# Performance work log

Measured on AMD Instinct MI355X. Metric: run time of the kernel, lower is better.

## Reference

```python
import jax, jax.numpy as jnp
import numpy as np

B, D, C, H, L = 32768, 64, 64, 1024, 6
EPS = 1e-5
NIN = (D - D // 2) + C  # unchanged half + cond = 96
SPLIT = D // 2          # 32


def setup_inputs() -> dict:
    key = jax.random.key(0)
    ks = jax.random.split(key, 12)
    s = 0.05
    return {
        "z": jax.random.normal(ks[0], (B, D), jnp.float32),
        "cond": jax.random.normal(ks[1], (B, C), jnp.float32),
        "W1": jax.random.normal(ks[2], (L, NIN, H), jnp.float32) * s,
        "b1": jax.random.normal(ks[3], (L, H), jnp.float32) * s,
        "W2": jax.random.normal(ks[4], (L, H, H), jnp.float32) * s,
        "b2": jax.random.normal(ks[5], (L, H), jnp.float32) * s,
        "Ws": jax.random.normal(ks[6], (L, H, SPLIT), jnp.float32) * s,
        "bs": jax.random.normal(ks[7], (L, SPLIT), jnp.float32) * s,
        "Wt": jax.random.normal(ks[8], (L, H, SPLIT), jnp.float32) * s,
        "bt": jax.random.normal(ks[9], (L, SPLIT), jnp.float32) * s,
        "bn_w": 1.0 + 0.1 * jax.random.normal(ks[10], (L, D), jnp.float32),
        "bn_b": 0.1 * jax.random.normal(ks[11], (L, D), jnp.float32),
    }


def reference(z, cond, W1, b1, W2, b2, Ws, bs, Wt, bt, bn_w, bn_b):
    x = z
    log_det = jnp.zeros((z.shape[0],), z.dtype)
    for i in range(L):
        # 'even' mask keeps even indices on even layers, odd indices otherwise
        if i % 2 == 0:
            keep, chg = np.arange(0, D, 2), np.arange(1, D, 2)
        else:
            keep, chg = np.arange(1, D, 2), np.arange(0, D, 2)
        # 2-layer MLP on [x_keep, cond]
        h = jax.nn.relu(jnp.concatenate([x[:, keep], cond], axis=1) @ W1[i] + b1[i])
        h = jax.nn.relu(h @ W2[i] + b2[i])
        log_s = jnp.tanh(h @ Ws[i] + bs[i])          # (B, SPLIT)
        t = h @ Wt[i] + bt[i]                         # (B, SPLIT)
        x2t = x[:, chg] * jnp.exp(log_s) + t
        x = jnp.zeros_like(x).at[:, keep].set(x[:, keep]).at[:, chg].set(x2t)
        log_det = log_det + log_s.sum(axis=1)
        # BatchNorm1d, training mode: batch mean / biased variance, eps=1e-5
        mean = x.mean(axis=0)
        var = x.var(axis=0)
        x = (x - mean) * jax.lax.rsqrt(var + EPS) * bn_w[i] + bn_b[i]
        log_det = log_det + jnp.log(jnp.abs(bn_w[i])).sum()
    return x, log_det
```

## Files before the change

### kernel.cpp

```cpp
#include <hip/hip_runtime.h>
#include <math.h>

#define BB 32768
#define DD 64
#define CC 64
#define HH 1024
#define LL 6
#define SPLIT 32
#define NIN 96
#define EPSV 1e-5f

typedef short short8 __attribute__((ext_vector_type(8)));
typedef float f32x4 __attribute__((ext_vector_type(4)));
typedef unsigned short u16;

__device__ __forceinline__ u16 f2bf(float f) {
    union { float f; unsigned int u; } c; c.f = f;
    unsigned int u = c.u + 0x7FFFu + ((c.u >> 16) & 1u);
    return (u16)(u >> 16);
}

__device__ __forceinline__ void gl_lds16(const u16* g, u16* l) {
    __builtin_amdgcn_global_load_lds(
        (const __attribute__((address_space(1))) unsigned int*)g,
        (__attribute__((address_space(3))) unsigned int*)l, 16, 0, 0);
}

__global__ void transpose_cvt_kernel(const float* __restrict__ src, u16* __restrict__ dst,
                                     int R, int C, int Rpad,
                                     long long sstride, long long dstride)
{
    __shared__ float tile[32][33];
    const float* s = src + (size_t)blockIdx.z * sstride;
    u16* d = dst + (size_t)blockIdx.z * dstride;
    int r0 = blockIdx.x * 32, c0 = blockIdx.y * 32;
    int tc = threadIdx.x & 31, tr = threadIdx.x >> 5;
#pragma unroll
    for (int i = 0; i < 4; ++i) {
        int r = r0 + tr + i * 8;
        tile[tr + i * 8][tc] = (r < R) ? s[(size_t)r * C + c0 + tc] : 0.f;
    }
    __syncthreads();
#pragma unroll
    for (int i = 0; i < 4; ++i) {
        int cc = tr + i * 8;
        d[(size_t)(c0 + cc) * Rpad + r0 + tc] = f2bf(tile[tc][cc]);
    }
}

__global__ __launch_bounds__(256)
void init_ain_cond_kernel(const float* __restrict__ cond, u16* __restrict__ Ain)
{
    int t = blockIdx.x * 256 + threadIdx.x;
    int c = t % 96, r = t / 96;
    Ain[(size_t)r * 128 + 32 + c] = (c < CC) ? f2bf(cond[(size_t)r * CC + c]) : (u16)0;
}

__global__ __launch_bounds__(256)
void build_keep_kernel(const float* __restrict__ x, u16* __restrict__ Ain, int keep_off)
{
    int t = blockIdx.x * 256 + threadIdx.x;
    int c = t & 31, r = t >> 5;
    Ain[(size_t)r * 128 + c] = f2bf(x[(size_t)r * DD + 2 * c + keep_off]);
}

__global__ __launch_bounds__(512, 2)
void gemm_tiled(const u16* __restrict__ A,
                const u16* __restrict__ Bt,
                const float* __restrict__ bias,
                u16* __restrict__ Cc,
                int K)
{
    __shared__ u16 sA[3][16 * 512];
    __shared__ u16 sB[3][16 * 512];

    const int t = threadIdx.x;
    const int w = t >> 6, lane = t & 63;
    const int lane16 = lane & 15, quad = lane >> 4;
    const int wm = w >> 2, wn = w & 3;

    int id = blockIdx.x;
    int nby = gridDim.x >> 2;
    int xcd = id & 7, slot = id >> 3;
    int bx = slot & 3, byq = slot >> 2;
    int by = xcd * (nby >> 3) + byq;
    const int bm = by * 256, bn = bx * 256;

    const int niter = K >> 5;

    auto stage = [&](int it, int buf) {
        int k0 = it * 32;
#pragma unroll
        for (int p = 0; p < 4; ++p) {
            int e = w + (p & 1) * 8;
            if (p < 2) {
                const u16* g = A + (size_t)(bm + e * 16 + lane16) * K + k0 + quad * 8;
                gl_lds16(g, &sA[buf][e * 512]);
            } else {
                const u16* g = Bt + (size_t)(bn + e * 16 + lane16) * K + k0 + quad * 8;
                gl_lds16(g, &sB[buf][e * 512]);
            }
        }
    };

    f32x4 acc[8][4];
#pragma unroll
    for (int a = 0; a < 8; ++a)
#pragma unroll
        for (int b = 0; b < 4; ++b) acc[a][b] = (f32x4){0.f, 0.f, 0.f, 0.f};

    const unsigned sAb = (unsigned)(size_t)(__attribute__((address_space(3))) u16*)&sA[0][0];
    const unsigned sBb = (unsigned)(size_t)(__attribute__((address_space(3))) u16*)&sB[0][0];
    const unsigned aoff = (unsigned)(wm * 8192 + lane * 16);
    const unsigned boff = (unsigned)(wn * 4096 + lane * 16);

    stage(0, 0);
    stage(1, 1);
    int buf = 0, sbuf = 2;
    for (int it = 0; it < niter; ++it) {
        asm volatile("s_waitcnt vmcnt(4)");
        __builtin_amdgcn_s_barrier();

        const unsigned aA = sAb + (unsigned)(buf * 16384) + aoff;
        const unsigned aB = sBb + (unsigned)(buf * 16384) + boff;
        short8 af[8], bf[4];
        asm volatile("ds_read_b128 %0, %1 offset:0"    : "=v"(bf[0]) : "v"(aB));
        asm volatile("ds_read_b128 %0, %1 offset:1024" : "=v"(bf[1]) : "v"(aB));
        asm volatile("ds_read_b128 %0, %1 offset:2048" : "=v"(bf[2]) : "v"(aB));
        asm volatile("ds_read_b128 %0, %1 offset:3072" : "=v"(bf[3]) : "v"(aB));
        asm volatile("ds_read_b128 %0, %1 offset:0"    : "=v"(af[0]) : "v"(aA));
        asm volatile("ds_read_b128 %0, %1 offset:1024" : "=v"(af[1]) : "v"(aA));
        asm volatile("ds_read_b128 %0, %1 offset:2048" : "=v"(af[2]) : "v"(aA));
        asm volatile("ds_read_b128 %0, %1 offset:3072" : "=v"(af[3]) : "v"(aA));
        asm volatile("ds_read_b128 %0, %1 offset:4096" : "=v"(af[4]) : "v"(aA));
        asm volatile("ds_read_b128 %0, %1 offset:5120" : "=v"(af[5]) : "v"(aA));
        asm volatile("ds_read_b128 %0, %1 offset:6144" : "=v"(af[6]) : "v"(aA));
        asm volatile("ds_read_b128 %0, %1 offset:7168" : "=v"(af[7]) : "v"(aA));

        if (it + 2 < niter)        stage(it + 2, sbuf);
        else if (it + 2 == niter)  stage(niter - 1, sbuf);

        asm volatile("s_waitcnt lgkmcnt(4)");
        __builtin_amdgcn_sched_barrier(0);
        __builtin_amdgcn_s_setprio(1);
#pragma unroll
        for (int a = 0; a < 4; ++a)
#pragma unroll
            for (int b = 0; b < 4; ++b)
                acc[a][b] = __builtin_amdgcn_mfma_f32_16x16x32_bf16(af[a], bf[b], acc[a][b], 0, 0, 0);
        __builtin_amdgcn_s_setprio(0);

        asm volatile("s_waitcnt lgkmcnt(0)");
        __builtin_amdgcn_sched_barrier(0);
        __builtin_amdgcn_s_setprio(1);
#pragma unroll
        for (int a = 4; a < 8; ++a)
#pragma unroll
            for (int b = 0; b < 4; ++b)
                acc[a][b] = __builtin_amdgcn_mfma_f32_16x16x32_bf16(af[a], bf[b], acc[a][b], 0, 0, 0);
        __builtin_amdgcn_s_setprio(0);

        buf  = (buf  == 2) ? 0 : buf  + 1;
        sbuf = (sbuf == 2) ? 0 : sbuf + 1;
    }
    __syncthreads();

    constexpr int ES = 72;
    float bv[4];
#pragma unroll
    for (int b = 0; b < 4; ++b) bv[b] = bias[bn + wn * 64 + b * 16 + lane16];
    u16* scr = ((u16*)sB) + w * (16 * ES);
#pragma unroll
    for (int a = 0; a < 8; ++a) {
#pragma unroll
        for (int b = 0; b < 4; ++b)
#pragma unroll
            for (int r = 0; r < 4; ++r) {
                float v = fmaxf(acc[a][b][r] + bv[b], 0.f);
                scr[(quad * 4 + r) * ES + b * 16 + lane16] = f2bf(v);
            }
#pragma unroll
        for (int ch = 0; ch < 2; ++ch) {
            int row = ch * 8 + (lane >> 3), colc = (lane & 7) * 8;
            short8 v = *(const short8*)(scr + row * ES + colc);
            *(short8*)(Cc + (size_t)(bm + wm * 128 + a * 16 + row) * 1024 + bn + wn * 64 + colc) = v;
        }
    }
}

__global__ __launch_bounds__(512)
void gemm3_coupling(const u16* __restrict__ A,
                    const u16* __restrict__ Bt,
                    const float* __restrict__ bs, const float* __restrict__ bt,
                    float* __restrict__ x, float* __restrict__ log_det,
                    float* __restrict__ stat_sum, float* __restrict__ stat_sumsq,
                    int keep_off, int row0)
{
    constexpr int ST_STRIDE = 66;
    __shared__ u16 stg[2][24 * 512];
    __shared__ float ssum[8][64], ssum2[8][64];
    float* sst = (float*)stg;

    const int t = threadIdx.x;
    const int w = t >> 6, lane = t & 63;
    const int lane16 = lane & 15, quad = lane >> 4;
    const int wm = w >> 1, wn = w & 1;
    const int bm = blockIdx.x * 128;

    auto stage = [&](int it, int buf) {
        int k0 = it * 64;
#pragma unroll
        for (int p = 0; p < 3; ++p) {
            int e = w + p * 8;
            if (e < 16) {
                int s = e >> 3, i = e & 7;
                const u16* g = A + (size_t)(bm + i * 16 + lane16) * HH + (k0 + s * 32 + quad * 8);
                gl_lds16(g, &stg[buf][e * 512]);
            } else {
                int j2 = e - 16, s = j2 >> 2, j = j2 & 3;
                const u16* g = Bt + (size_t)(j * 16 + lane16) * HH + (k0 + s * 32 + quad * 8);
                gl_lds16(g, &stg[buf][e * 512]);
            }
        }
    };

    f32x4 acc[2][2];
#pragma unroll
    for (int a = 0; a < 2; ++a)
#pragma unroll
        for (int b = 0; b < 2; ++b) acc[a][b] = (f32x4){0.f, 0.f, 0.f, 0.f};

    stage(0, 0);
    for (int it = 0; it < 16; ++it) {
        const int buf = it & 1;
        __syncthreads();
        if (it + 1 < 16) stage(it + 1, buf ^ 1);
        u16* ldsA = stg[buf];
        u16* ldsB = stg[buf] + 16 * 512;
#pragma unroll
        for (int s = 0; s < 2; ++s) {
            short8 af[2], bfr[2];
#pragma unroll
            for (int a = 0; a < 2; ++a)
                af[a] = *(const short8*)(ldsA + ((s * 8 + wm * 2 + a) * 512) + lane * 8);
#pragma unroll
            for (int b = 0; b < 2; ++b)
                bfr[b] = *(const short8*)(ldsB + ((s * 4 + wn * 2 + b) * 512) + lane * 8);
#pragma unroll
            for (int a = 0; a < 2; ++a)
#pragma unroll
                for (int b = 0; b < 2; ++b)
                    acc[a][b] = __builtin_amdgcn_mfma_f32_16x16x32_bf16(af[a], bfr[b], acc[a][b], 0, 0, 0);
        }
    }
    __syncthreads();

#pragma unroll
    for (int a = 0; a < 2; ++a)
#pragma unroll
        for (int b = 0; b < 2; ++b)
#pragma unroll
            for (int r = 0; r < 4; ++r) {
                int row = wm * 32 + a * 16 + quad * 4 + r;
                int col = wn * 32 + b * 16 + lane16;
                sst[row * ST_STRIDE + col] = acc[a][b][r];
            }
    __syncthreads();

    const int f = lane;
    const bool is_chg = ((f & 1) != keep_off);
    const int j = f >> 1;
    float bsj = 0.f, btj = 0.f;
    if (is_chg) { bsj = bs[j]; btj = bt[j]; }

    float lsum = 0.f, lsum2 = 0.f;
    for (int i = 0; i < 16; ++i) {
        int crow = w * 16 + i;
        int grow = row0 + bm + crow;
        float xv = x[(size_t)grow * DD + f];
        float ld = 0.f;
        if (is_chg) {
            float s_raw = sst[crow * ST_STRIDE + j];
            float t_raw = sst[crow * ST_STRIDE + SPLIT + j];
            float ls = tanhf(s_raw + bsj);
            float tv = t_raw + btj;
            xv = xv * expf(ls) + tv;
            x[(size_t)grow * DD + f] = xv;
            ld = ls;
        }
        for (int off = 32; off > 0; off >>= 1) ld += __shfl_down(ld, off, 64);
        if (f == 0) log_det[grow] += ld;
        lsum  += xv;
        lsum2 += xv * xv;
    }

    ssum[w][f]  = lsum;
    ssum2[w][f] = lsum2;
    __syncthreads();
    if (t < 64) {
        float a = 0.f, b = 0.f;
#pragma unroll
        for (int g = 0; g < 8; ++g) { a += ssum[g][t]; b += ssum2[g][t]; }
        atomicAdd(stat_sum + t, a);
        atomicAdd(stat_sumsq + t, b);
    }
}

__global__ __launch_bounds__(256)
void normalize_kernel(const float* __restrict__ xin, float* __restrict__ xout,
                      const float* __restrict__ stat_sum, const float* __restrict__ stat_sumsq,
                      const float* __restrict__ bn_w, const float* __restrict__ bn_b,
                      float* __restrict__ log_det,
                      u16* __restrict__ Ain, int off_next)
{
    __shared__ float sscale[64], sshift[64], scsum;
    int t = threadIdx.x;
    if (t < 64) {
        const float invB = 1.f / (float)BB;
        float mean = stat_sum[t] * invB;
        float var  = stat_sumsq[t] * invB - mean * mean;
        float inv  = rsqrtf(var + EPSV);
        float wv   = bn_w[t];
        float sc   = inv * wv;
        sscale[t] = sc;
        sshift[t] = bn_b[t] - mean * sc;
        float lg = logf(fabsf(wv));
        for (int off = 32; off > 0; off >>= 1) lg += __shfl_down(lg, off, 64);
        if (t == 0) scsum = lg;
    }
    __syncthreads();

    int idx = blockIdx.x * blockDim.x + t;
    int f0 = (idx & 15) * 4;
    int row = idx >> 4;
    float4 v = ((const float4*)xin)[idx];
    v.x = v.x * sscale[f0 + 0] + sshift[f0 + 0];
    v.y = v.y * sscale[f0 + 1] + sshift[f0 + 1];
    v.z = v.z * sscale[f0 + 2] + sshift[f0 + 2];
    v.w = v.w * sscale[f0 + 3] + sshift[f0 + 3];
    ((float4*)xout)[idx] = v;
    if ((idx & 15) == 0) log_det[row] += scsum;
    if (Ain) {
        float a0 = off_next ? v.y : v.x;
        float a1 = off_next ? v.w : v.z;
        ushort2 u; u.x = f2bf(a0); u.y = f2bf(a1);
        *(ushort2*)(Ain + (size_t)row * 128 + (f0 >> 1)) = u;
    }
}

extern "C" void kernel_launch(void* const* d_in, const int* in_sizes, int n_in,
                              void* d_out, int out_size, void* d_ws, size_t ws_size,
                              hipStream_t stream)
{
    const float* z    = (const float*)d_in[0];
    const float* cond = (const float*)d_in[1];
    const float* W1   = (const float*)d_in[2];
    const float* b1   = (const float*)d_in[3];
    const float* W2   = (const float*)d_in[4];
    const float* b2   = (const float*)d_in[5];
    const float* Ws   = (const float*)d_in[6];
    const float* bs   = (const float*)d_in[7];
    const float* Wt   = (const float*)d_in[8];
    const float* bt   = (const float*)d_in[9];
    const float* bn_w = (const float*)d_in[10];
    const float* bn_b = (const float*)d_in[11];

    float* out_x  = (float*)d_out;
    float* out_ld = out_x + (size_t)BB * DD;

    char* p = (char*)d_ws;
    size_t used = 0;
    auto alloc = [&](size_t bytes) { void* q = p + used; used += (bytes + 255) & ~(size_t)255; return q; };

    float* xbuf = (float*)alloc((size_t)BB * DD * 4);
    u16*   w1t  = (u16*)alloc((size_t)LL * HH * 128 * 2);
    u16*   w2t  = (u16*)alloc((size_t)LL * HH * HH * 2);
    u16*   wstt = (u16*)alloc((size_t)LL * 64 * HH * 2);
    u16*   Ain  = (u16*)alloc((size_t)BB * 128 * 2);
    float* stat_sum   = (float*)alloc(64 * 4);
    float* stat_sumsq = (float*)alloc(64 * 4);

    int CH = BB;
    while (CH > 8192 && used + (size_t)CH * 4096 + 4096 > ws_size) CH >>= 1;
    u16* h1 = (u16*)alloc((size_t)CH * HH * 2);
    u16* h2 = (u16*)alloc((size_t)CH * HH * 2);

    hipMemcpyAsync(xbuf, z, (size_t)BB * DD * sizeof(float), hipMemcpyDeviceToDevice, stream);
    hipMemsetAsync(out_ld, 0, (size_t)BB * sizeof(float), stream);

    transpose_cvt_kernel<<<dim3(128/32, HH/32, LL), 256, 0, stream>>>(
        W1, w1t, NIN, HH, 128, (long long)NIN * HH, (long long)HH * 128);
    transpose_cvt_kernel<<<dim3(HH/32, HH/32, LL), 256, 0, stream>>>(
        W2, w2t, HH, HH, HH, (long long)HH * HH, (long long)HH * HH);
    transpose_cvt_kernel<<<dim3(HH/32, SPLIT/32, LL), 256, 0, stream>>>(
        Ws, wstt, HH, SPLIT, HH, (long long)HH * SPLIT, (long long)64 * HH);
    transpose_cvt_kernel<<<dim3(HH/32, SPLIT/32, LL), 256, 0, stream>>>(
        Wt, wstt + (size_t)SPLIT * HH, HH, SPLIT, HH, (long long)HH * SPLIT, (long long)64 * HH);

    init_ain_cond_kernel<<<BB * 96 / 256, 256, 0, stream>>>(cond, Ain);
    build_keep_kernel<<<BB * 32 / 256, 256, 0, stream>>>(xbuf, Ain, 0);

    for (int l = 0; l < LL; ++l) {
        const int off = l & 1;
        hipMemsetAsync(stat_sum, 0, 2 * 64 * sizeof(float), stream);

        for (int c = 0; c < BB / CH; ++c) {
            const int row0 = c * CH;

            gemm_tiled<<<(CH / 256) * 4, 512, 0, stream>>>(
                Ain + (size_t)row0 * 128, w1t + (size_t)l * HH * 128,
                b1 + (size_t)l * HH, h1, 128);

            gemm_tiled<<<(CH / 256) * 4, 512, 0, stream>>>(
                h1, w2t + (size_t)l * HH * HH,
                b2 + (size_t)l * HH, h2, HH);

            gemm3_coupling<<<CH / 128, 512, 0, stream>>>(
                h2, wstt + (size_t)l * 64 * HH,
                bs + (size_t)l * SPLIT, bt + (size_t)l * SPLIT,
                xbuf, out_ld, stat_sum, stat_sumsq, off, row0);
        }

        float* xout = (l == LL - 1) ? out_x : xbuf;
        u16* ain_next = (l < LL - 1) ? Ain : nullptr;
        normalize_kernel<<<(BB * DD / 4) / 256, 256, 0, stream>>>(
            xbuf, xout, stat_sum, stat_sumsq,
            bn_w + (size_t)l * DD, bn_b + (size_t)l * DD,
            out_ld, ain_next, (l + 1) & 1);
    }
}
```

Before: 952.7 us.

## Software-pipeline LDS fragment reads across iterations with three-stage prefetch

Restructures the GEMM main loop so it prefetches three stages up front. Each iteration reads the next tile's first half of A and B fragments into registers while the second half of the current MFMAs runs, and the barrier moves to mid-iteration. The goal is to hide LDS read latency and the per-iteration barrier stall behind MFMA work. In exchange it needs extra registers for the next-tile fragments and adds a redundant final stage of the last tile, which could lower occupancy or cause spills.

```diff
diff --git a/kernel.cpp b/kernel.cpp
--- a/kernel.cpp
+++ b/kernel.cpp
@@ -116,30 +116,35 @@
 
     stage(0, 0);
     stage(1, 1);
-    int buf = 0, sbuf = 2;
+    stage(2, 2);
+    asm volatile("s_waitcnt vmcnt(8)");
+    __builtin_amdgcn_s_barrier();
+
+    short8 af[8], bf[4], naf[4], nbf[4];
+    {
+        const unsigned aA = sAb + aoff, aB = sBb + boff;
+        asm volatile("ds_read_b128 %0, %1 offset:0"    : "=&v"(bf[0]) : "v"(aB));
+        asm volatile("ds_read_b128 %0, %1 offset:1024" : "=&v"(bf[1]) : "v"(aB));
+        asm volatile("ds_read_b128 %0, %1 offset:2048" : "=&v"(bf[2]) : "v"(aB));
+        asm volatile("ds_read_b128 %0, %1 offset:3072" : "=&v"(bf[3]) : "v"(aB));
+        asm volatile("ds_read_b128 %0, %1 offset:0"    : "=&v"(af[0]) : "v"(aA));
+        asm volatile("ds_read_b128 %0, %1 offset:1024" : "=&v"(af[1]) : "v"(aA));
+        asm volatile("ds_read_b128 %0, %1 offset:2048" : "=&v"(af[2]) : "v"(aA));
+        asm volatile("ds_read_b128 %0, %1 offset:3072" : "=&v"(af[3]) : "v"(aA));
+    }
+
+    unsigned co = 0;
+    int sb = 0;
     for (int it = 0; it < niter; ++it) {
-        asm volatile("s_waitcnt vmcnt(4)");
-        __builtin_amdgcn_s_barrier();
-
-        const unsigned aA = sAb + (unsigned)(buf * 16384) + aoff;
-        const unsigned aB = sBb + (unsigned)(buf * 16384) + boff;
-        short8 af[8], bf[4];
-        asm volatile("ds_read_b128 %0, %1 offset:0"    : "=v"(bf[0]) : "v"(aB));
-        asm volatile("ds_read_b128 %0, %1 offset:1024" : "=v"(bf[1]) : "v"(aB));
-        asm volatile("ds_read_b128 %0, %1 offset:2048" : "=v"(bf[2]) : "v"(aB));
-        asm volatile("ds_read_b128 %0, %1 offset:3072" : "=v"(bf[3]) : "v"(aB));
-        asm volatile("ds_read_b128 %0, %1 offset:0"    : "=v"(af[0]) : "v"(aA));
-        asm volatile("ds_read_b128 %0, %1 offset:1024" : "=v"(af[1]) : "v"(aA));
-        asm volatile("ds_read_b128 %0, %1 offset:2048" : "=v"(af[2]) : "v"(aA));
-        asm volatile("ds_read_b128 %0, %1 offset:3072" : "=v"(af[3]) : "v"(aA));
-        asm volatile("ds_read_b128 %0, %1 offset:4096" : "=v"(af[4]) : "v"(aA));
-        asm volatile("ds_read_b128 %0, %1 offset:5120" : "=v"(af[5]) : "v"(aA));
-        asm volatile("ds_read_b128 %0, %1 offset:6144" : "=v"(af[6]) : "v"(aA));
-        asm volatile("ds_read_b128 %0, %1 offset:7168" : "=v"(af[7]) : "v"(aA));
-
-        if (it + 2 < niter)        stage(it + 2, sbuf);
-        else if (it + 2 == niter)  stage(niter - 1, sbuf);
-
+        const unsigned no = (co == 32768u) ? 0u : co + 16384u;
+
+        {
+            const unsigned aA = sAb + co + aoff;
+            asm volatile("ds_read_b128 %0, %1 offset:4096" : "=&v"(af[4]) : "v"(aA));
+            asm volatile("ds_read_b128 %0, %1 offset:5120" : "=&v"(af[5]) : "v"(aA));
+            asm volatile("ds_read_b128 %0, %1 offset:6144" : "=&v"(af[6]) : "v"(aA));
+            asm volatile("ds_read_b128 %0, %1 offset:7168" : "=&v"(af[7]) : "v"(aA));
+        }
         asm volatile("s_waitcnt lgkmcnt(4)");
         __builtin_amdgcn_sched_barrier(0);
         __builtin_amdgcn_s_setprio(1);
@@ -150,7 +155,23 @@
                 acc[a][b] = __builtin_amdgcn_mfma_f32_16x16x32_bf16(af[a], bf[b], acc[a][b], 0, 0, 0);
         __builtin_amdgcn_s_setprio(0);
 
-        asm volatile("s_waitcnt lgkmcnt(0)");
+        asm volatile("s_waitcnt vmcnt(4) lgkmcnt(0)");
+        __builtin_amdgcn_s_barrier();
+        __builtin_amdgcn_sched_barrier(0);
+
+        if (it + 1 < niter) {
+            const unsigned aA = sAb + no + aoff, aB = sBb + no + boff;
+            asm volatile("ds_read_b128 %0, %1 offset:0"    : "=&v"(nbf[0]) : "v"(aB));
+            asm volatile("ds_read_b128 %0, %1 offset:1024" : "=&v"(nbf[1]) : "v"(aB));
+            asm volatile("ds_read_b128 %0, %1 offset:2048" : "=&v"(nbf[2]) : "v"(aB));
+            asm volatile("ds_read_b128 %0, %1 offset:3072" : "=&v"(nbf[3]) : "v"(aB));
+            asm volatile("ds_read_b128 %0, %1 offset:0"    : "=&v"(naf[0]) : "v"(aA));
+            asm volatile("ds_read_b128 %0, %1 offset:1024" : "=&v"(naf[1]) : "v"(aA));
+            asm volatile("ds_read_b128 %0, %1 offset:2048" : "=&v"(naf[2]) : "v"(aA));
+            asm volatile("ds_read_b128 %0, %1 offset:3072" : "=&v"(naf[3]) : "v"(aA));
+        }
+        if (it + 3 < niter)       stage(it + 3, sb);
+        else if (it + 1 < niter)  stage(niter - 1, sb);
         __builtin_amdgcn_sched_barrier(0);
         __builtin_amdgcn_s_setprio(1);
 #pragma unroll
@@ -160,8 +181,10 @@
                 acc[a][b] = __builtin_amdgcn_mfma_f32_16x16x32_bf16(af[a], bf[b], acc[a][b], 0, 0, 0);
         __builtin_amdgcn_s_setprio(0);
 
-        buf  = (buf  == 2) ? 0 : buf  + 1;
-        sbuf = (sbuf == 2) ? 0 : sbuf + 1;
+#pragma unroll
+        for (int i = 0; i < 4; ++i) { af[i] = naf[i]; bf[i] = nbf[i]; }
+        co = no;
+        sb = (sb == 2) ? 0 : sb + 1;
     }
     __syncthreads();
 
```

Measured after the change: 970.1 us. About the same (+1.8%).

## Restructure GEMM main loop into 64-wide K tiles with interleaved half-stage prefetch

Applied to the files above, without the earlier changes.

Replaces the triple-buffered 32-wide K pipeline with a double-buffered 64-wide K tile. Each tile is split into four sub-phases that interleave LDS fragment reads, quarter-sized global-to-LDS prefetches of the next tile, and MFMA blocks, with barriers between them. The aim is to spread global loads across the compute and overlap them with MFMA, while halving loop iterations. In exchange it adds many more barriers per iteration and relies on careful vmcnt accounting to stay correct.

```diff
diff --git a/kernel.cpp b/kernel.cpp
--- a/kernel.cpp
+++ b/kernel.cpp
@@ -26,6 +26,9 @@
         (__attribute__((address_space(3))) unsigned int*)l, 16, 0, 0);
 }
 
+#define DSR(dst, addr, off) \
+    asm volatile("ds_read_b128 %0, %1 offset:" #off : "=&v"(dst) : "v"(addr))
+
 __global__ void transpose_cvt_kernel(const float* __restrict__ src, u16* __restrict__ dst,
                                      int R, int C, int Rpad,
                                      long long sstride, long long dstride)
@@ -71,8 +74,8 @@
                 u16* __restrict__ Cc,
                 int K)
 {
-    __shared__ u16 sA[3][16 * 512];
-    __shared__ u16 sB[3][16 * 512];
+    __shared__ u16 sA[2][32 * 512];
+    __shared__ u16 sB[2][32 * 512];
 
     const int t = threadIdx.x;
     const int w = t >> 6, lane = t & 63;
@@ -86,18 +89,19 @@
     int by = xcd * (nby >> 3) + byq;
     const int bm = by * 256, bn = bx * 256;
 
-    const int niter = K >> 5;
-
-    auto stage = [&](int it, int buf) {
-        int k0 = it * 32;
-#pragma unroll
-        for (int p = 0; p < 4; ++p) {
-            int e = w + (p & 1) * 8;
-            if (p < 2) {
-                const u16* g = A + (size_t)(bm + e * 16 + lane16) * K + k0 + quad * 8;
+    const int ntile = K >> 6;
+
+    auto stage_half = [&](int kt, int op, int s, int buf) {
+        int k0 = kt * 64 + s * 32 + quad * 8;
+#pragma unroll
+        for (int r = 0; r < 2; ++r) {
+            int i = r * 8 + w;
+            int e = s * 16 + i;
+            if (op == 0) {
+                const u16* g = A + (size_t)(bm + i * 16 + lane16) * K + k0;
                 gl_lds16(g, &sA[buf][e * 512]);
             } else {
-                const u16* g = Bt + (size_t)(bn + e * 16 + lane16) * K + k0 + quad * 8;
+                const u16* g = Bt + (size_t)(bn + i * 16 + lane16) * K + k0;
                 gl_lds16(g, &sB[buf][e * 512]);
             }
         }
@@ -111,36 +115,33 @@
 
     const unsigned sAb = (unsigned)(size_t)(__attribute__((address_space(3))) u16*)&sA[0][0];
     const unsigned sBb = (unsigned)(size_t)(__attribute__((address_space(3))) u16*)&sB[0][0];
-    const unsigned aoff = (unsigned)(wm * 8192 + lane * 16);
-    const unsigned boff = (unsigned)(wn * 4096 + lane * 16);
-
-    stage(0, 0);
-    stage(1, 1);
-    int buf = 0, sbuf = 2;
-    for (int it = 0; it < niter; ++it) {
-        asm volatile("s_waitcnt vmcnt(4)");
-        __builtin_amdgcn_s_barrier();
-
-        const unsigned aA = sAb + (unsigned)(buf * 16384) + aoff;
-        const unsigned aB = sBb + (unsigned)(buf * 16384) + boff;
-        short8 af[8], bf[4];
-        asm volatile("ds_read_b128 %0, %1 offset:0"    : "=v"(bf[0]) : "v"(aB));
-        asm volatile("ds_read_b128 %0, %1 offset:1024" : "=v"(bf[1]) : "v"(aB));
-        asm volatile("ds_read_b128 %0, %1 offset:2048" : "=v"(bf[2]) : "v"(aB));
-        asm volatile("ds_read_b128 %0, %1 offset:3072" : "=v"(bf[3]) : "v"(aB));
-        asm volatile("ds_read_b128 %0, %1 offset:0"    : "=v"(af[0]) : "v"(aA));
-        asm volatile("ds_read_b128 %0, %1 offset:1024" : "=v"(af[1]) : "v"(aA));
-        asm volatile("ds_read_b128 %0, %1 offset:2048" : "=v"(af[2]) : "v"(aA));
-        asm volatile("ds_read_b128 %0, %1 offset:3072" : "=v"(af[3]) : "v"(aA));
-        asm volatile("ds_read_b128 %0, %1 offset:4096" : "=v"(af[4]) : "v"(aA));
-        asm volatile("ds_read_b128 %0, %1 offset:5120" : "=v"(af[5]) : "v"(aA));
-        asm volatile("ds_read_b128 %0, %1 offset:6144" : "=v"(af[6]) : "v"(aA));
-        asm volatile("ds_read_b128 %0, %1 offset:7168" : "=v"(af[7]) : "v"(aA));
-
-        if (it + 2 < niter)        stage(it + 2, sbuf);
-        else if (it + 2 == niter)  stage(niter - 1, sbuf);
-
-        asm volatile("s_waitcnt lgkmcnt(4)");
+    const unsigned aoff = (unsigned)(wm * 8 * 1024 + lane * 16);
+    const unsigned boff = (unsigned)(wn * 4 * 1024 + lane * 16);
+
+    stage_half(0, 0, 0, 0);
+    stage_half(0, 1, 0, 0);
+    stage_half(0, 0, 1, 0);
+    stage_half(0, 1, 1, 0);
+    asm volatile("s_waitcnt vmcnt(4)");
+    __builtin_amdgcn_s_barrier();
+
+    short8 af[4], ag[4], bf[4], bg[4];
+    for (int kt = 0; kt < ntile; ++kt) {
+        const unsigned base = (unsigned)((kt & 1) << 15);
+        const unsigned aA0 = sAb + base + aoff;
+        const unsigned aB0 = sBb + base + boff;
+        const unsigned aA1 = aA0 + 16384;
+        const unsigned aB1 = aB0 + 16384;
+        const int nk = (kt + 1 < ntile) ? kt + 1 : kt;
+        const int nb = (kt + 1) & 1;
+
+        DSR(bf[0], aB0, 0); DSR(bf[1], aB0, 1024);
+        DSR(bf[2], aB0, 2048); DSR(bf[3], aB0, 3072);
+        DSR(af[0], aA0, 0); DSR(af[1], aA0, 1024);
+        DSR(af[2], aA0, 2048); DSR(af[3], aA0, 3072);
+        stage_half(nk, 0, 0, nb);
+        __builtin_amdgcn_s_barrier();
+        asm volatile("s_waitcnt lgkmcnt(0)");
         __builtin_amdgcn_sched_barrier(0);
         __builtin_amdgcn_s_setprio(1);
 #pragma unroll
@@ -149,19 +150,56 @@
             for (int b = 0; b < 4; ++b)
                 acc[a][b] = __builtin_amdgcn_mfma_f32_16x16x32_bf16(af[a], bf[b], acc[a][b], 0, 0, 0);
         __builtin_amdgcn_s_setprio(0);
-
+        __builtin_amdgcn_s_barrier();
+
+        DSR(ag[0], aA0, 4096); DSR(ag[1], aA0, 5120);
+        DSR(ag[2], aA0, 6144); DSR(ag[3], aA0, 7168);
+        stage_half(nk, 1, 0, nb);
+        __builtin_amdgcn_s_barrier();
         asm volatile("s_waitcnt lgkmcnt(0)");
         __builtin_amdgcn_sched_barrier(0);
         __builtin_amdgcn_s_setprio(1);
 #pragma unroll
-        for (int a = 4; a < 8; ++a)
+        for (int a = 0; a < 4; ++a)
 #pragma unroll
             for (int b = 0; b < 4; ++b)
-                acc[a][b] = __builtin_amdgcn_mfma_f32_16x16x32_bf16(af[a], bf[b], acc[a][b], 0, 0, 0);
+                acc[4 + a][b] = __builtin_amdgcn_mfma_f32_16x16x32_bf16(ag[a], bf[b], acc[4 + a][b], 0, 0, 0);
         __builtin_amdgcn_s_setprio(0);
-
-        buf  = (buf  == 2) ? 0 : buf  + 1;
-        sbuf = (sbuf == 2) ? 0 : sbuf + 1;
+        asm volatile("s_waitcnt vmcnt(4)");
+        __builtin_amdgcn_s_barrier();
+
+        DSR(bg[0], aB1, 0); DSR(bg[1], aB1, 1024);
+        DSR(bg[2], aB1, 2048); DSR(bg[3], aB1, 3072);
+        DSR(af[0], aA1, 0); DSR(af[1], aA1, 1024);
+        DSR(af[2], aA1, 2048); DSR(af[3], aA1, 3072);
+        stage_half(nk, 0, 1, nb);
+        __builtin_amdgcn_s_barrier();
+        asm volatile("s_waitcnt lgkmcnt(0)");
+        __builtin_amdgcn_sched_barrier(0);
+        __builtin_amdgcn_s_setprio(1);
+#pragma unroll
+        for (int a = 0; a < 4; ++a)
+#pragma unroll
+            for (int b = 0; b < 4; ++b)
+                acc[a][b] = __builtin_amdgcn_mfma_f32_16x16x32_bf16(af[a], bg[b], acc[a][b], 0, 0, 0);
+        __builtin_amdgcn_s_setprio(0);
+        __builtin_amdgcn_s_barrier();
+
+        DSR(ag[0], aA1, 4096); DSR(ag[1], aA1, 5120);
+        DSR(ag[2], aA1, 6144); DSR(ag[3], aA1, 7168);
+        stage_half(nk, 1, 1, nb);
+        __builtin_amdgcn_s_barrier();
+        asm volatile("s_waitcnt lgkmcnt(0)");
+        __builtin_amdgcn_sched_barrier(0);
+        __builtin_amdgcn_s_setprio(1);
+#pragma unroll
+        for (int a = 0; a < 4; ++a)
+#pragma unroll
+            for (int b = 0; b < 4; ++b)
+                acc[4 + a][b] = __builtin_amdgcn_mfma_f32_16x16x32_bf16(ag[a], bg[b], acc[4 + a][b], 0, 0, 0);
+        __builtin_amdgcn_s_setprio(0);
+        asm volatile("s_waitcnt vmcnt(4)");
+        __builtin_amdgcn_s_barrier();
     }
     __syncthreads();
 
```

Result: no change. 961.2 us (+0.9%).

## Load B fragments directly to registers and double-buffer 64-wide A tiles in LDS

Applied to the files above, without the earlier changes.

The main GEMM stops staging the B (weight) operand through LDS. Each wave now loads its B fragments straight from global memory into registers, prefetched one tile ahead. A is staged in 64-wide K tiles with two buffers instead of three 32-wide buffers, which halves the number of barriers per K step and removes the LDS traffic for B. The trade-offs are more VGPR pressure from holding two sets of B registers, redundant global reads of B across the wm wave rows, and vmcnt(0) waits that may expose global latency.

```diff
diff --git a/kernel.cpp b/kernel.cpp
--- a/kernel.cpp
+++ b/kernel.cpp
@@ -26,6 +26,9 @@
         (__attribute__((address_space(3))) unsigned int*)l, 16, 0, 0);
 }
 
+#define DSRO(dst, addr, off) \
+    asm volatile("ds_read_b128 %0, %1 offset:%2" : "=&v"(dst) : "v"(addr), "i"(off))
+
 __global__ void transpose_cvt_kernel(const float* __restrict__ src, u16* __restrict__ dst,
                                      int R, int C, int Rpad,
                                      long long sstride, long long dstride)
@@ -62,6 +65,57 @@
     int t = blockIdx.x * 256 + threadIdx.x;
     int c = t & 31, r = t >> 5;
     Ain[(size_t)r * 128 + c] = f2bf(x[(size_t)r * DD + 2 * c + keep_off]);
+}
+
+template<int BASE>
+__device__ __forceinline__ void k_tile(const unsigned lA, f32x4 (&acc)[8][4],
+                                       const short8 (&b0)[4], const short8 (&b1)[4])
+{
+    short8 af[4], ag[4];
+    DSRO(af[0], lA, BASE + 0);    DSRO(af[1], lA, BASE + 1024);
+    DSRO(af[2], lA, BASE + 2048); DSRO(af[3], lA, BASE + 3072);
+    DSRO(ag[0], lA, BASE + 4096); DSRO(ag[1], lA, BASE + 5120);
+    DSRO(ag[2], lA, BASE + 6144); DSRO(ag[3], lA, BASE + 7168);
+    asm volatile("s_waitcnt lgkmcnt(4)");
+    __builtin_amdgcn_sched_barrier(0);
+    __builtin_amdgcn_s_setprio(1);
+#pragma unroll
+    for (int a = 0; a < 4; ++a)
+#pragma unroll
+        for (int b = 0; b < 4; ++b)
+            acc[a][b] = __builtin_amdgcn_mfma_f32_16x16x32_bf16(af[a], b0[b], acc[a][b], 0, 0, 0);
+    __builtin_amdgcn_s_setprio(0);
+    DSRO(af[0], lA, BASE + 16384); DSRO(af[1], lA, BASE + 17408);
+    DSRO(af[2], lA, BASE + 18432); DSRO(af[3], lA, BASE + 19456);
+    asm volatile("s_waitcnt lgkmcnt(4)");
+    __builtin_amdgcn_sched_barrier(0);
+    __builtin_amdgcn_s_setprio(1);
+#pragma unroll
+    for (int a = 0; a < 4; ++a)
+#pragma unroll
+        for (int b = 0; b < 4; ++b)
+            acc[4 + a][b] = __builtin_amdgcn_mfma_f32_16x16x32_bf16(ag[a], b0[b], acc[4 + a][b], 0, 0, 0);
+    __builtin_amdgcn_s_setprio(0);
+    DSRO(ag[0], lA, BASE + 20480); DSRO(ag[1], lA, BASE + 21504);
+    DSRO(ag[2], lA, BASE + 22528); DSRO(ag[3], lA, BASE + 23552);
+    asm volatile("s_waitcnt lgkmcnt(4)");
+    __builtin_amdgcn_sched_barrier(0);
+    __builtin_amdgcn_s_setprio(1);
+#pragma unroll
+    for (int a = 0; a < 4; ++a)
+#pragma unroll
+        for (int b = 0; b < 4; ++b)
+            acc[a][b] = __builtin_amdgcn_mfma_f32_16x16x32_bf16(af[a], b1[b], acc[a][b], 0, 0, 0);
+    __builtin_amdgcn_s_setprio(0);
+    asm volatile("s_waitcnt lgkmcnt(0)");
+    __builtin_amdgcn_sched_barrier(0);
+    __builtin_amdgcn_s_setprio(1);
+#pragma unroll
+    for (int a = 0; a < 4; ++a)
+#pragma unroll
+        for (int b = 0; b < 4; ++b)
+            acc[4 + a][b] = __builtin_amdgcn_mfma_f32_16x16x32_bf16(ag[a], b1[b], acc[4 + a][b], 0, 0, 0);
+    __builtin_amdgcn_s_setprio(0);
 }
 
 __global__ __launch_bounds__(512, 2)
@@ -71,8 +125,7 @@
                 u16* __restrict__ Cc,
                 int K)
 {
-    __shared__ u16 sA[3][16 * 512];
-    __shared__ u16 sB[3][16 * 512];
+    __shared__ u16 sA[2][32 * 512];
 
     const int t = threadIdx.x;
     const int w = t >> 6, lane = t & 63;
@@ -86,23 +139,29 @@
     int by = xcd * (nby >> 3) + byq;
     const int bm = by * 256, bn = bx * 256;
 
-    const int niter = K >> 5;
-
-    auto stage = [&](int it, int buf) {
-        int k0 = it * 32;
-#pragma unroll
-        for (int p = 0; p < 4; ++p) {
-            int e = w + (p & 1) * 8;
-            if (p < 2) {
-                const u16* g = A + (size_t)(bm + e * 16 + lane16) * K + k0 + quad * 8;
-                gl_lds16(g, &sA[buf][e * 512]);
-            } else {
-                const u16* g = Bt + (size_t)(bn + e * 16 + lane16) * K + k0 + quad * 8;
-                gl_lds16(g, &sB[buf][e * 512]);
-            }
+    const int ntile = K >> 6;
+
+    auto stage_tile = [&](int kt2, int buf) {
+        const u16* Abase = A + (size_t)(bm + lane16) * K + quad * 8 + (size_t)kt2 * 64;
+#pragma unroll
+        for (int r = 0; r < 4; ++r) {
+            int e = r * 8 + w;
+            int s = e >> 4, i = e & 15;
+            const u16* g = Abase + (size_t)(i * 16) * K + s * 32;
+            gl_lds16(g, &sA[buf][e * 512]);
         }
     };
 
+    const u16* Bbase = Bt + (size_t)(bn + wn * 64 + lane16) * K + quad * 8;
+    auto loadB = [&](int kt2, short8 (&b0)[4], short8 (&b1)[4]) {
+#pragma unroll
+        for (int j = 0; j < 4; ++j) {
+            const u16* p = Bbase + (size_t)(j * 16) * K + (size_t)kt2 * 64;
+            b0[j] = *(const short8*)p;
+            b1[j] = *(const short8*)(p + 32);
+        }
+    };
+
     f32x4 acc[8][4];
 #pragma unroll
     for (int a = 0; a < 8; ++a)
@@ -110,58 +169,30 @@
         for (int b = 0; b < 4; ++b) acc[a][b] = (f32x4){0.f, 0.f, 0.f, 0.f};
 
     const unsigned sAb = (unsigned)(size_t)(__attribute__((address_space(3))) u16*)&sA[0][0];
-    const unsigned sBb = (unsigned)(size_t)(__attribute__((address_space(3))) u16*)&sB[0][0];
-    const unsigned aoff = (unsigned)(wm * 8192 + lane * 16);
-    const unsigned boff = (unsigned)(wn * 4096 + lane * 16);
-
-    stage(0, 0);
-    stage(1, 1);
-    int buf = 0, sbuf = 2;
-    for (int it = 0; it < niter; ++it) {
-        asm volatile("s_waitcnt vmcnt(4)");
+    const unsigned lA  = sAb + (unsigned)(wm * 8192 + lane * 16);
+
+    short8 bA0[4], bA1[4], bB0[4], bB1[4];
+
+    stage_tile(0, 0);
+    loadB(0, bA0, bA1);
+    asm volatile("s_waitcnt vmcnt(0)");
+    __builtin_amdgcn_s_barrier();
+
+    const int npair = ntile >> 1;
+    for (int tp = 0; tp < npair; ++tp) {
+        const int kt = tp << 1;
+        loadB(kt + 1, bB0, bB1);
+        stage_tile(kt + 1, 1);
+        k_tile<0>(lA, acc, bA0, bA1);
+        asm volatile("s_waitcnt vmcnt(0)");
         __builtin_amdgcn_s_barrier();
-
-        const unsigned aA = sAb + (unsigned)(buf * 16384) + aoff;
-        const unsigned aB = sBb + (unsigned)(buf * 16384) + boff;
-        short8 af[8], bf[4];
-        asm volatile("ds_read_b128 %0, %1 offset:0"    : "=v"(bf[0]) : "v"(aB));
-        asm volatile("ds_read_b128 %0, %1 offset:1024" : "=v"(bf[1]) : "v"(aB));
-        asm volatile("ds_read_b128 %0, %1 offset:2048" : "=v"(bf[2]) : "v"(aB));
-        asm volatile("ds_read_b128 %0, %1 offset:3072" : "=v"(bf[3]) : "v"(aB));
-        asm volatile("ds_read_b128 %0, %1 offset:0"    : "=v"(af[0]) : "v"(aA));
-        asm volatile("ds_read_b128 %0, %1 offset:1024" : "=v"(af[1]) : "v"(aA));
-        asm volatile("ds_read_b128 %0, %1 offset:2048" : "=v"(af[2]) : "v"(aA));
-        asm volatile("ds_read_b128 %0, %1 offset:3072" : "=v"(af[3]) : "v"(aA));
-        asm volatile("ds_read_b128 %0, %1 offset:4096" : "=v"(af[4]) : "v"(aA));
-        asm volatile("ds_read_b128 %0, %1 offset:5120" : "=v"(af[5]) : "v"(aA));
-        asm volatile("ds_read_b128 %0, %1 offset:6144" : "=v"(af[6]) : "v"(aA));
-        asm volatile("ds_read_b128 %0, %1 offset:7168" : "=v"(af[7]) : "v"(aA));
-
-        if (it + 2 < niter)        stage(it + 2, sbuf);
-        else if (it + 2 == niter)  stage(niter - 1, sbuf);
-
-        asm volatile("s_waitcnt lgkmcnt(4)");
-        __builtin_amdgcn_sched_barrier(0);
-        __builtin_amdgcn_s_setprio(1);
-#pragma unroll
-        for (int a = 0; a < 4; ++a)
-#pragma unroll
-            for (int b = 0; b < 4; ++b)
-                acc[a][b] = __builtin_amdgcn_mfma_f32_16x16x32_bf16(af[a], bf[b], acc[a][b], 0, 0, 0);
-        __builtin_amdgcn_s_setprio(0);
-
-        asm volatile("s_waitcnt lgkmcnt(0)");
-        __builtin_amdgcn_sched_barrier(0);
-        __builtin_amdgcn_s_setprio(1);
-#pragma unroll
-        for (int a = 4; a < 8; ++a)
-#pragma unroll
-            for (int b = 0; b < 4; ++b)
-                acc[a][b] = __builtin_amdgcn_mfma_f32_16x16x32_bf16(af[a], bf[b], acc[a][b], 0, 0, 0);
-        __builtin_amdgcn_s_setprio(0);
-
-        buf  = (buf  == 2) ? 0 : buf  + 1;
-        sbuf = (sbuf == 2) ? 0 : sbuf + 1;
+        if (kt + 2 < ntile) {
+            loadB(kt + 2, bA0, bA1);
+            stage_tile(kt + 2, 0);
+        }
+        k_tile<32768>(lA, acc, bB0, bB1);
+        asm volatile("s_waitcnt vmcnt(0)");
+        __builtin_amdgcn_s_barrier();
     }
     __syncthreads();
 
@@ -169,7 +200,7 @@
     float bv[4];
 #pragma unroll
     for (int b = 0; b < 4; ++b) bv[b] = bias[bn + wn * 64 + b * 16 + lane16];
-    u16* scr = ((u16*)sB) + w * (16 * ES);
+    u16* scr = ((u16*)sA) + w * (16 * ES);
 #pragma unroll
     for (int a = 0; a < 8; ++a) {
 #pragma unroll
```

Measured after the change: 1.748 ms. +83.5%, slower.
